# Performance work log

Hardware: AMD Instinct MI355X
Metric: run time of the kernel (lower is better)

The kernel has to match this reference:

```python
import jax, jax.numpy as jnp
import numpy as np

H, W, C_IN, C_ADD = 721, 1440, 78, 8
N_NODES, K = 5882, 128
DAY_OF_YEAR = 182.5  # module default time_of_year
LN_EPS = 1e-5        # haiku LayerNorm default
NORM_EPS = 1e-7


def setup_inputs() -> dict:
    key = jax.random.key(0)
    ks = jax.random.split(key, 4)
    return {
        "var_grid": jax.random.normal(ks[0], (H, W, C_IN), dtype=jnp.float32),
        "nearby_idx": jax.random.randint(ks[1], (N_NODES, K), 0, H * W),
        "input_means": jnp.zeros((C_IN + C_ADD,), jnp.float32),
        "input_stds": jnp.ones((C_IN + C_ADD,), jnp.float32),
        "W1": jax.random.normal(ks[2], (C_IN + C_ADD, 256), dtype=jnp.float32) * 0.1,
        "b1": jnp.zeros((256,), jnp.float32),
        "ln_scale": jnp.ones((256,), jnp.float32),
        "ln_offset": jnp.zeros((256,), jnp.float32),
        "W2": jax.random.normal(ks[3], (256, 256), dtype=jnp.float32) * 0.1,
        "b2": jnp.zeros((256,), jnp.float32),
    }


def _additional_features(h, w):
    # 8 extra channels: sin/cos of lat/lon, normalized day-of-year, 3 zero pads
    lat = jnp.linspace(-90.0, 90.0, h)
    lon = jnp.linspace(0.0, 360.0, w)
    lat2d = jnp.broadcast_to(lat[:, None], (h, w))
    lon2d = jnp.broadcast_to(lon[None, :], (h, w))
    lat_r, lon_r = jnp.radians(lat2d), jnp.radians(lon2d)
    day = jnp.float32(DAY_OF_YEAR / 365.0)
    z = jnp.zeros((h, w), jnp.float32)
    return jnp.stack([
        jnp.sin(lat_r), jnp.cos(lat_r), jnp.sin(lon_r), jnp.cos(lon_r),
        jnp.full((h, w), day, jnp.float32), z, z, z,
    ], axis=-1)  # [H, W, 8]


def reference(var_grid, nearby_idx, input_means, input_stds,
              W1, b1, ln_scale, ln_offset, W2, b2):
    h, w, c = var_grid.shape
    add = _additional_features(h, w)                       # [H, W, 8]
    flat = jnp.concatenate([var_grid, add], -1).reshape(h * w, c + C_ADD)
    gathered = flat[nearby_idx]                            # [N, K, 86] irregular gather
    x = (gathered - input_means) / (input_stds + NORM_EPS)
    hidden = jax.nn.relu(jnp.einsum('nkc,cd->nkd', x, W1) + b1)
    mu = hidden.mean(-1, keepdims=True)
    var = hidden.var(-1, keepdims=True)
    hidden = (hidden - mu) * jax.lax.rsqrt(var + LN_EPS) * ln_scale + ln_offset
    nodes = jnp.einsum('nkd,de->nke', hidden, W2) + b2     # [N, K, 256]
    return nodes
```

## Files before the change

kernel.cpp:

```cpp
#include <hip/hip_runtime.h>
#include <hip/hip_bf16.h>
#include <math.h>

#define GH 721
#define GW 1440
#define C_IN 78
#define C_TOT 86
#define NNODES 5882
#define KNEIGH 128
#define M_TOTAL (NNODES * KNEIGH)
#define TM 64
#define NBLOCKS (M_TOTAL / TM)

typedef __attribute__((ext_vector_type(8))) short bf16x8;
typedef __attribute__((ext_vector_type(4))) float f32x4;

__device__ __forceinline__ unsigned short f2bf(float x) {
    __hip_bfloat16 b = __float2bfloat16(x);
    union { __hip_bfloat16 h; unsigned short u; } cv; cv.h = b; return cv.u;
}

__global__ void prep_kernel(const float* __restrict__ W1, const float* __restrict__ W2,
                            const float* __restrict__ means, const float* __restrict__ stds,
                            unsigned short* __restrict__ bp1, unsigned short* __restrict__ bp2,
                            float* __restrict__ latT, float* __restrict__ lonT,
                            float* __restrict__ nrm)
{
    const int NB1 = 3 * 4 * 256 * 8;
    const int NB2 = 8 * 4 * 256 * 8;
    const int NTOT = NB1 + NB2 + GH + GW + C_TOT;
    for (int e = blockIdx.x * blockDim.x + threadIdx.x; e < NTOT;
         e += gridDim.x * blockDim.x) {
        if (e < NB1) {
            int j = e & 7, c = (e >> 3) & 255, o = (e >> 11) & 3, s = e >> 13;
            int k = s * 32 + o * 8 + j;
            float v = (k < C_TOT) ? W1[k * 256 + c] : 0.f;
            bp1[e] = f2bf(v);
        } else if (e < NB1 + NB2) {
            int t = e - NB1;
            int j = t & 7, c = (t >> 3) & 255, o = (t >> 11) & 3, s = t >> 13;
            int k = s * 32 + o * 8 + j;
            bp2[t] = f2bf(W2[k * 256 + c]);
        } else if (e < NB1 + NB2 + GH) {
            int h = e - NB1 - NB2;
            float r = (-90.f + 0.25f * (float)h) * 0.017453292519943295f;
            latT[2 * h]     = (sinf(r) - means[78]) / (stds[78] + 1e-7f);
            latT[2 * h + 1] = (cosf(r) - means[79]) / (stds[79] + 1e-7f);
        } else if (e < NB1 + NB2 + GH + GW) {
            int w = e - NB1 - NB2 - GH;
            float r = ((float)w * (360.f / 1439.f)) * 0.017453292519943295f;
            lonT[2 * w]     = (sinf(r) - means[80]) / (stds[80] + 1e-7f);
            lonT[2 * w + 1] = (cosf(r) - means[81]) / (stds[81] + 1e-7f);
        } else {
            int c = e - NB1 - NB2 - GH - GW;
            nrm[c] = means[c];
            nrm[C_TOT + c] = 1.f / (stds[c] + 1e-7f);
        }
    }
}

__global__ __launch_bounds__(256, 2)
void fused_kernel(const float* __restrict__ var_grid, const int* __restrict__ idxs,
                  const unsigned short* __restrict__ bp1, const unsigned short* __restrict__ bp2,
                  const float* __restrict__ latT, const float* __restrict__ lonT,
                  const float* __restrict__ nrm,
                  const float* __restrict__ b1, const float* __restrict__ lnS,
                  const float* __restrict__ lnO, const float* __restrict__ b2,
                  float* __restrict__ out)
{
    __shared__ unsigned short x_lds[TM][104];
    __shared__ unsigned short h_lds[TM * 256];
    __shared__ float red[2][4][TM];
    __shared__ float nM[C_TOT], nI[C_TOT];
    __shared__ int idx_s[TM];

    const int tid  = threadIdx.x;
    const int lane = tid & 63;
    const int wave = tid >> 6;
    const int l15  = lane & 15;
    const int lg   = lane >> 4;
    const int wbase = wave * 64;
    const long block0 = (long)blockIdx.x * TM;

    for (int c = tid; c < C_TOT; c += 256) { nM[c] = nrm[c]; nI[c] = nrm[C_TOT + c]; }
    if (tid < TM) idx_s[tid] = idxs[block0 + tid];
    __syncthreads();

    {
        const int row = tid >> 2, p = tid & 3;
        const int idx = idx_s[row];
        const int hh = idx / GW;
        const int ww = idx - hh * GW;
        const float* src = var_grid + (long)idx * C_IN;
        unsigned int* xrow = (unsigned int*)&x_lds[row][0];
        #pragma unroll 4
        for (int q = p; q < 48; q += 4) {
            const int c = 2 * q;
            float v0, v1;
            if (q < 39) {
                float2 t2 = *(const float2*)(src + c);
                v0 = (t2.x - nM[c]) * nI[c];
                v1 = (t2.y - nM[c + 1]) * nI[c + 1];
            } else if (q == 39) { v0 = latT[2 * hh]; v1 = latT[2 * hh + 1]; }
            else if (q == 40)   { v0 = lonT[2 * ww]; v1 = lonT[2 * ww + 1]; }
            else if (q == 41)   { v0 = (0.5f - nM[82]) * nI[82]; v1 = (0.f - nM[83]) * nI[83]; }
            else if (q == 42)   { v0 = (0.f - nM[84]) * nI[84];  v1 = (0.f - nM[85]) * nI[85]; }
            else { v0 = 0.f; v1 = 0.f; }
            xrow[q] = ((unsigned int)f2bf(v1) << 16) | (unsigned int)f2bf(v0);
        }
    }
    __syncthreads();

    f32x4 acc[4][4];
    #pragma unroll
    for (int mf = 0; mf < 4; ++mf)
        #pragma unroll
        for (int nf = 0; nf < 4; ++nf) acc[mf][nf] = (f32x4){0.f, 0.f, 0.f, 0.f};

    #pragma unroll
    for (int s = 0; s < 3; ++s) {
        bf16x8 af[4], bw[4];
        #pragma unroll
        for (int mf = 0; mf < 4; ++mf)
            af[mf] = *(const bf16x8*)&x_lds[mf * 16 + l15][s * 32 + lg * 8];
        #pragma unroll
        for (int nf = 0; nf < 4; ++nf)
            bw[nf] = *(const bf16x8*)(bp1 + ((size_t)((s * 4 + lg) * 256) + wbase + nf * 16 + l15) * 8);
        #pragma unroll
        for (int mf = 0; mf < 4; ++mf)
            #pragma unroll
            for (int nf = 0; nf < 4; ++nf)
                acc[mf][nf] = __builtin_amdgcn_mfma_f32_16x16x32_bf16(af[mf], bw[nf], acc[mf][nf], 0, 0, 0);
    }

    float b1v[4], lsv[4], lov[4], b2v[4];
    #pragma unroll
    for (int nf = 0; nf < 4; ++nf) {
        int col = wbase + nf * 16 + l15;
        b1v[nf] = b1[col]; lsv[nf] = lnS[col]; lov[nf] = lnO[col]; b2v[nf] = b2[col];
    }

    float sm[4][4], sq[4][4];
    #pragma unroll
    for (int mf = 0; mf < 4; ++mf)
        #pragma unroll
        for (int i = 0; i < 4; ++i) { sm[mf][i] = 0.f; sq[mf][i] = 0.f; }

    #pragma unroll
    for (int mf = 0; mf < 4; ++mf)
        #pragma unroll
        for (int nf = 0; nf < 4; ++nf)
            #pragma unroll
            for (int i = 0; i < 4; ++i) {
                float v = fmaxf(acc[mf][nf][i] + b1v[nf], 0.f);
                acc[mf][nf][i] = v;
                sm[mf][i] += v;
                sq[mf][i] += v * v;
            }

    #pragma unroll
    for (int m = 1; m < 16; m <<= 1)
        #pragma unroll
        for (int mf = 0; mf < 4; ++mf)
            #pragma unroll
            for (int i = 0; i < 4; ++i) {
                sm[mf][i] += __shfl_xor(sm[mf][i], m, 64);
                sq[mf][i] += __shfl_xor(sq[mf][i], m, 64);
            }

    if (l15 == 0) {
        #pragma unroll
        for (int mf = 0; mf < 4; ++mf)
            #pragma unroll
            for (int i = 0; i < 4; ++i) {
                int row = mf * 16 + lg * 4 + i;
                red[0][wave][row] = sm[mf][i];
                red[1][wave][row] = sq[mf][i];
            }
    }
    __syncthreads();

    #pragma unroll
    for (int mf = 0; mf < 4; ++mf)
        #pragma unroll
        for (int i = 0; i < 4; ++i) {
            int row = mf * 16 + lg * 4 + i;
            float tot = red[0][0][row] + red[0][1][row] + red[0][2][row] + red[0][3][row];
            float tq  = red[1][0][row] + red[1][1][row] + red[1][2][row] + red[1][3][row];
            float mean = tot * (1.f / 256.f);
            float var  = tq * (1.f / 256.f) - mean * mean;
            float rs = rsqrtf(var + 1e-5f);
            #pragma unroll
            for (int nf = 0; nf < 4; ++nf) {
                float v = (acc[mf][nf][i] - mean) * rs * lsv[nf] + lov[nf];
                int col = wbase + nf * 16 + l15;
                unsigned off = (unsigned)(row * 512 + col * 2);
                off ^= (unsigned)((row & 7) << 4);
                *(unsigned short*)((char*)h_lds + off) = f2bf(v);
            }
        }
    __syncthreads();

    #pragma unroll
    for (int mf = 0; mf < 4; ++mf)
        #pragma unroll
        for (int nf = 0; nf < 4; ++nf) acc[mf][nf] = (f32x4){0.f, 0.f, 0.f, 0.f};

    #pragma unroll
    for (int s = 0; s < 8; ++s) {
        bf16x8 af[4], bw[4];
        #pragma unroll
        for (int mf = 0; mf < 4; ++mf) {
            int row = mf * 16 + l15;
            unsigned off = (unsigned)(row * 512 + (s * 32 + lg * 8) * 2);
            off ^= (unsigned)((row & 7) << 4);
            af[mf] = *(const bf16x8*)((char*)h_lds + off);
        }
        #pragma unroll
        for (int nf = 0; nf < 4; ++nf)
            bw[nf] = *(const bf16x8*)(bp2 + ((size_t)((s * 4 + lg) * 256) + wbase + nf * 16 + l15) * 8);
        #pragma unroll
        for (int mf = 0; mf < 4; ++mf)
            #pragma unroll
            for (int nf = 0; nf < 4; ++nf)
                acc[mf][nf] = __builtin_amdgcn_mfma_f32_16x16x32_bf16(af[mf], bw[nf], acc[mf][nf], 0, 0, 0);
    }

    #pragma unroll
    for (int mf = 0; mf < 4; ++mf)
        #pragma unroll
        for (int i = 0; i < 4; ++i) {
            long row_g = block0 + mf * 16 + lg * 4 + i;
            float* po = out + row_g * 256 + wbase;
            #pragma unroll
            for (int nf = 0; nf < 4; ++nf)
                po[nf * 16 + l15] = acc[mf][nf][i] + b2v[nf];
        }
}

extern "C" void kernel_launch(void* const* d_in, const int* in_sizes, int n_in,
                              void* d_out, int out_size, void* d_ws, size_t ws_size,
                              hipStream_t stream) {
    const float* var_grid = (const float*)d_in[0];
    const int*   idxs     = (const int*)d_in[1];
    const float* means    = (const float*)d_in[2];
    const float* stds     = (const float*)d_in[3];
    const float* W1       = (const float*)d_in[4];
    const float* b1       = (const float*)d_in[5];
    const float* lnS      = (const float*)d_in[6];
    const float* lnO      = (const float*)d_in[7];
    const float* W2       = (const float*)d_in[8];
    const float* b2       = (const float*)d_in[9];
    float* out = (float*)d_out;

    char* ws = (char*)d_ws;
    unsigned short* bp1 = (unsigned short*)ws;
    unsigned short* bp2 = (unsigned short*)(ws + 49152);
    float* latT = (float*)(ws + 180224);
    float* lonT = (float*)(ws + 186000);
    float* nrm  = (float*)(ws + 197520);

    prep_kernel<<<362, 256, 0, stream>>>(W1, W2, means, stds, bp1, bp2, latT, lonT, nrm);
    fused_kernel<<<NBLOCKS, 256, 0, stream>>>(var_grid, idxs, bp1, bp2, latT, lonT, nrm,
                                              b1, lnS, lnO, b2, out);
}
```

Baseline: 487.2 us.

## Fold input normalization into W1 and bias, alias x tile onto h LDS

Moves the per-channel mean/std normalization out of the gather loop by scaling W1 rows by 1/std and folding the means, the constant day-of-year feature and b1 into a precomputed bias. The x tile now aliases the h_lds buffer, and the idx/normalization LDS staging and its barrier are removed. Launch bounds go from 2 to 4 blocks per SU to raise occupancy, and the bias loads are hoisted ahead of the first GEMM. The cost is extra prep work with a serial 86-step loop per column, a different bf16 rounding point for normalized values, and register pressure under the tighter launch bound.

```diff
diff --git a/kernel.cpp b/kernel.cpp
--- a/kernel.cpp
+++ b/kernel.cpp
@@ -5,7 +5,6 @@
 #define GH 721
 #define GW 1440
 #define C_IN 78
-#define C_TOT 86
 #define NNODES 5882
 #define KNEIGH 128
 #define M_TOTAL (NNODES * KNEIGH)
@@ -22,19 +21,21 @@
 
 __global__ void prep_kernel(const float* __restrict__ W1, const float* __restrict__ W2,
                             const float* __restrict__ means, const float* __restrict__ stds,
+                            const float* __restrict__ b1,
                             unsigned short* __restrict__ bp1, unsigned short* __restrict__ bp2,
                             float* __restrict__ latT, float* __restrict__ lonT,
-                            float* __restrict__ nrm)
+                            float* __restrict__ b1p)
 {
     const int NB1 = 3 * 4 * 256 * 8;
     const int NB2 = 8 * 4 * 256 * 8;
-    const int NTOT = NB1 + NB2 + GH + GW + C_TOT;
+    const int NTOT = NB1 + NB2 + GH + GW + 256;
     for (int e = blockIdx.x * blockDim.x + threadIdx.x; e < NTOT;
          e += gridDim.x * blockDim.x) {
         if (e < NB1) {
             int j = e & 7, c = (e >> 3) & 255, o = (e >> 11) & 3, s = e >> 13;
             int k = s * 32 + o * 8 + j;
-            float v = (k < C_TOT) ? W1[k * 256 + c] : 0.f;
+            float v = 0.f;
+            if (k < 82) v = W1[k * 256 + c] / (stds[k] + 1e-7f);
             bp1[e] = f2bf(v);
         } else if (e < NB1 + NB2) {
             int t = e - NB1;
@@ -44,35 +45,39 @@
         } else if (e < NB1 + NB2 + GH) {
             int h = e - NB1 - NB2;
             float r = (-90.f + 0.25f * (float)h) * 0.017453292519943295f;
-            latT[2 * h]     = (sinf(r) - means[78]) / (stds[78] + 1e-7f);
-            latT[2 * h + 1] = (cosf(r) - means[79]) / (stds[79] + 1e-7f);
+            latT[2 * h]     = sinf(r);
+            latT[2 * h + 1] = cosf(r);
         } else if (e < NB1 + NB2 + GH + GW) {
             int w = e - NB1 - NB2 - GH;
             float r = ((float)w * (360.f / 1439.f)) * 0.017453292519943295f;
-            lonT[2 * w]     = (sinf(r) - means[80]) / (stds[80] + 1e-7f);
-            lonT[2 * w + 1] = (cosf(r) - means[81]) / (stds[81] + 1e-7f);
+            lonT[2 * w]     = sinf(r);
+            lonT[2 * w + 1] = cosf(r);
         } else {
             int c = e - NB1 - NB2 - GH - GW;
-            nrm[c] = means[c];
-            nrm[C_TOT + c] = 1.f / (stds[c] + 1e-7f);
-        }
-    }
-}
-
-__global__ __launch_bounds__(256, 2)
+            float acc = b1[c];
+            #pragma unroll 1
+            for (int k = 0; k < 86; ++k) {
+                float inv = 1.f / (stds[k] + 1e-7f);
+                float w = W1[k * 256 + c] * inv;
+                acc -= means[k] * w;
+                if (k == 82) acc += 0.5f * w;
+            }
+            b1p[c] = acc;
+        }
+    }
+}
+
+__global__ __launch_bounds__(256, 4)
 void fused_kernel(const float* __restrict__ var_grid, const int* __restrict__ idxs,
                   const unsigned short* __restrict__ bp1, const unsigned short* __restrict__ bp2,
                   const float* __restrict__ latT, const float* __restrict__ lonT,
-                  const float* __restrict__ nrm,
-                  const float* __restrict__ b1, const float* __restrict__ lnS,
+                  const float* __restrict__ b1p, const float* __restrict__ lnS,
                   const float* __restrict__ lnO, const float* __restrict__ b2,
                   float* __restrict__ out)
 {
-    __shared__ unsigned short x_lds[TM][104];
     __shared__ unsigned short h_lds[TM * 256];
     __shared__ float red[2][4][TM];
-    __shared__ float nM[C_TOT], nI[C_TOT];
-    __shared__ int idx_s[TM];
+    unsigned short (*x_lds)[104] = (unsigned short (*)[104])h_lds;
 
     const int tid  = threadIdx.x;
     const int lane = tid & 63;
@@ -82,32 +87,32 @@
     const int wbase = wave * 64;
     const long block0 = (long)blockIdx.x * TM;
 
-    for (int c = tid; c < C_TOT; c += 256) { nM[c] = nrm[c]; nI[c] = nrm[C_TOT + c]; }
-    if (tid < TM) idx_s[tid] = idxs[block0 + tid];
-    __syncthreads();
-
     {
         const int row = tid >> 2, p = tid & 3;
-        const int idx = idx_s[row];
+        const int idx = idxs[block0 + row];
         const int hh = idx / GW;
         const int ww = idx - hh * GW;
         const float* src = var_grid + (long)idx * C_IN;
         unsigned int* xrow = (unsigned int*)&x_lds[row][0];
-        #pragma unroll 4
-        for (int q = p; q < 48; q += 4) {
-            const int c = 2 * q;
+        #pragma unroll
+        for (int t = 0; t < 12; ++t) {
+            const int q = p + 4 * t;
             float v0, v1;
             if (q < 39) {
-                float2 t2 = *(const float2*)(src + c);
-                v0 = (t2.x - nM[c]) * nI[c];
-                v1 = (t2.y - nM[c + 1]) * nI[c + 1];
+                float2 t2 = *(const float2*)(src + 2 * q);
+                v0 = t2.x; v1 = t2.y;
             } else if (q == 39) { v0 = latT[2 * hh]; v1 = latT[2 * hh + 1]; }
             else if (q == 40)   { v0 = lonT[2 * ww]; v1 = lonT[2 * ww + 1]; }
-            else if (q == 41)   { v0 = (0.5f - nM[82]) * nI[82]; v1 = (0.f - nM[83]) * nI[83]; }
-            else if (q == 42)   { v0 = (0.f - nM[84]) * nI[84];  v1 = (0.f - nM[85]) * nI[85]; }
-            else { v0 = 0.f; v1 = 0.f; }
+            else                { v0 = 0.f; v1 = 0.f; }
             xrow[q] = ((unsigned int)f2bf(v1) << 16) | (unsigned int)f2bf(v0);
         }
+    }
+
+    float b1v[4], lsv[4], lov[4], b2v[4];
+    #pragma unroll
+    for (int nf = 0; nf < 4; ++nf) {
+        int col = wbase + nf * 16 + l15;
+        b1v[nf] = b1p[col]; lsv[nf] = lnS[col]; lov[nf] = lnO[col]; b2v[nf] = b2[col];
     }
     __syncthreads();
 
@@ -131,13 +136,6 @@
             #pragma unroll
             for (int nf = 0; nf < 4; ++nf)
                 acc[mf][nf] = __builtin_amdgcn_mfma_f32_16x16x32_bf16(af[mf], bw[nf], acc[mf][nf], 0, 0, 0);
-    }
-
-    float b1v[4], lsv[4], lov[4], b2v[4];
-    #pragma unroll
-    for (int nf = 0; nf < 4; ++nf) {
-        int col = wbase + nf * 16 + l15;
-        b1v[nf] = b1[col]; lsv[nf] = lnS[col]; lov[nf] = lnO[col]; b2v[nf] = b2[col];
     }
 
     float sm[4][4], sq[4][4];
@@ -258,9 +256,9 @@
     unsigned short* bp2 = (unsigned short*)(ws + 49152);
     float* latT = (float*)(ws + 180224);
     float* lonT = (float*)(ws + 186000);
-    float* nrm  = (float*)(ws + 197520);
-
-    prep_kernel<<<362, 256, 0, stream>>>(W1, W2, means, stds, bp1, bp2, latT, lonT, nrm);
-    fused_kernel<<<NBLOCKS, 256, 0, stream>>>(var_grid, idxs, bp1, bp2, latT, lonT, nrm,
-                                              b1, lnS, lnO, b2, out);
-}
+    float* b1p  = (float*)(ws + 197520);
+
+    prep_kernel<<<362, 256, 0, stream>>>(W1, W2, means, stds, b1, bp1, bp2, latT, lonT, b1p);
+    fused_kernel<<<NBLOCKS, 256, 0, stream>>>(var_grid, idxs, bp1, bp2, latT, lonT,
+                                              b1p, lnS, lnO, b2, out);
+}
```

Result: slower. 564.3 us (+15.8%).
